# Kernel tuning notes

Measured on AMD Instinct MI355X. Metric: run time of the kernel, lower is better.

## Reference

```python
import jax, jax.numpy as jnp
import numpy as np

N_XI = 512      # internal REN state dim
L = 128         # nonlinearity channels (sequential loop length)
N_STATES = 128  # plant state dim (w)
N_INPUTS = 64   # control input dim (u)
EPS = 0.001
STD = 0.1
BATCH = 32768


def _model_params(X, Y):
    """set_model_param(): derive constrained REN matrices from free params X, Y."""
    n, l = N_XI, L
    H = X.T @ X + EPS * jnp.eye(2 * n + l, dtype=X.dtype)
    H11 = H[:n, :n]
    H21 = H[n:n + l, :n]
    H22 = H[n:n + l, n:n + l]
    H31 = H[n + l:, :n]
    H32 = H[n + l:, n:n + l]
    H33 = H[n + l:, n + l:]
    Fm = H31                                 # (n_xi, n_xi)
    B1 = H32                                 # (n_xi, l)
    E = 0.5 * (H11 + H33 + Y - Y.T)          # (n_xi, n_xi)
    Lam = 0.5 * jnp.diag(H22)                # (l,) strictly positive
    D11 = -jnp.tril(H22, -1)                 # strictly lower triangular (l, l)
    C1 = -H21                                # (l, n_xi)
    return Fm, B1, E, Lam, D11, C1


def setup_inputs() -> dict:
    key = jax.random.key(0)
    ks = jax.random.split(key, 9)
    n, l = N_XI, L
    return {
        "t": 0,
        "w": jax.random.normal(ks[0], (BATCH, 1, N_STATES), jnp.float32),
        "xi": jax.random.normal(ks[1], (BATCH, 1, n), jnp.float32),
        "X": jax.random.normal(ks[2], (2 * n + l, 2 * n + l), jnp.float32) * STD,
        "Y": jax.random.normal(ks[3], (n, n), jnp.float32) * STD,
        "B2": jax.random.normal(ks[4], (n, N_STATES), jnp.float32) * STD,
        "C2": jax.random.normal(ks[5], (N_INPUTS, n), jnp.float32) * STD,
        "D21": jax.random.normal(ks[6], (N_INPUTS, l), jnp.float32) * STD,
        "D22": jax.random.normal(ks[7], (N_INPUTS, N_STATES), jnp.float32) * STD,
        "D12": jax.random.normal(ks[8], (l, N_STATES), jnp.float32) * STD,
    }


def reference(t, w, xi, X, Y, B2, C2, D21, D22, D12):
    Fm, B1, E, Lam, D11, C1 = _model_params(X, Y)
    w2 = w[:, 0, :]    # (B, num_states)
    xi2 = xi[:, 0, :]  # (B, n_xi)

    # Precompute the xi- and w-dependent parts of every row's pre-activation.
    pre = xi2 @ C1.T + w2 @ D12.T  # (B, l)

    eye = jnp.eye(L, dtype=pre.dtype)

    def step(eps, xs):
        # Sequential forward substitution: row i only reads eps[:, :i]
        # because D11 is strictly lower triangular.
        d_row, p_col, lam, e_row = xs
        v = p_col + eps @ d_row            # (B,)
        e = jnp.tanh(v / lam)
        return eps + e[:, None] * e_row[None, :], None

    eps0 = jnp.zeros_like(pre)
    epsilon, _ = jax.lax.scan(step, eps0, (D11, pre.T, Lam, eye))  # (B, l)

    E_xi = xi2 @ Fm.T + epsilon @ B1.T + w2 @ B2.T      # (B, n_xi)
    xi_ = E_xi @ jnp.linalg.inv(E).T                    # (B, n_xi)
    u = xi2 @ C2.T + epsilon @ D21.T + w2 @ D22.T       # (B, num_inputs)
    return u[:, None, :], xi_[:, None, :]
```

## Files before the change

kernel.cpp:

```cpp
#include <hip/hip_runtime.h>
#include <cstddef>

#define NXI   512
#define LL    128
#define NST   128
#define NU    64
#define BATCH 32768
#define TW    1152
#define EPSC  0.001f
#define KC    768
#define NC    576
#define NCP   640

typedef unsigned short u16;
typedef __attribute__((ext_vector_type(8))) short   short8;
typedef __attribute__((ext_vector_type(4))) short   short4v;
typedef __attribute__((ext_vector_type(4))) float   f32x4;

__device__ __forceinline__ u16 f2bf(float f) {
    unsigned u = __float_as_uint(f);
    u += 0x7FFFu + ((u >> 16) & 1u);
    return (u16)(u >> 16);
}

__global__ __launch_bounds__(256) void k_setup(const float* __restrict__ X, u16* __restrict__ XT,
                                               const float* __restrict__ xi, const float* __restrict__ w,
                                               u16* __restrict__ Ac) {
    __shared__ float t[32][33];
    int blk = blockIdx.x;
    if (blk < 1296) {
        int tx = threadIdx.x & 31, ty = threadIdx.x >> 5;
        int bx = blk % 36, by = blk / 36;
        #pragma unroll
        for (int q = 0; q < 4; q++) {
            int r = ty + q * 8;
            t[r][tx] = X[(size_t)(by * 32 + r) * TW + bx * 32 + tx];
        }
        __syncthreads();
        #pragma unroll
        for (int q = 0; q < 4; q++) {
            int r = ty + q * 8;
            XT[(size_t)(bx * 32 + r) * TW + by * 32 + tx] = f2bf(t[tx][r]);
        }
        return;
    }
    size_t tt = (size_t)(blk - 1296) * 256 + threadIdx.x;
    int b = (int)(tt / 80), ch = (int)(tt % 80);
    const float* src;
    int col;
    if (ch < 64) { src = xi + (size_t)b * NXI + ch * 8;        col = ch * 8; }
    else         { src = w  + (size_t)b * NST + (ch - 64) * 8; col = 640 + (ch - 64) * 8; }
    f32x4 a = ((const f32x4*)src)[0], c = ((const f32x4*)src)[1];
    short8 o;
    o[0]=(short)f2bf(a[0]); o[1]=(short)f2bf(a[1]); o[2]=(short)f2bf(a[2]); o[3]=(short)f2bf(a[3]);
    o[4]=(short)f2bf(c[0]); o[5]=(short)f2bf(c[1]); o[6]=(short)f2bf(c[2]); o[7]=(short)f2bf(c[3]);
    *(short8*)(Ac + (size_t)b * KC + col) = o;
}

__global__ __launch_bounds__(256) void k_gemm2(const u16* __restrict__ A, int lda,
                                               const u16* __restrict__ W, int ldw,
                                               float* __restrict__ C0, int ldc0, int nsplit,
                                               float* __restrict__ C1, int ldc1,
                                               int K, int nbx, int ntrue, int swz) {
    __shared__ __align__(16) u16 As[2][128 * 32];
    __shared__ __align__(16) u16 Bs[2][128 * 32];
    int id = blockIdx.x;
    int bx, by;
    if (swz) {
        int j = id >> 3;
        int per = (int)(gridDim.x >> 3) / nbx;
        by = (id & 7) * per + j / nbx;
        bx = j - (j / nbx) * nbx;
    } else {
        by = id / nbx;
        bx = id - by * nbx;
    }
    const int tid = threadIdx.x;
    const int wave = tid >> 6, lane = tid & 63, quad = lane >> 4, l16 = lane & 15;
    const int bm0 = by * 128, bn0 = bx * 128;
    const int srow = tid >> 2;
    const int sch = (((tid & 3) ^ ((srow >> 2) & 3))) * 8;
    const u16* ga0 = A + (size_t)(bm0 + srow) * lda + sch;
    const u16* ga1 = ga0 + (size_t)64 * lda;
    const u16* gb0 = W + (size_t)(bn0 + srow) * ldw + sch;
    const u16* gb1 = gb0 + (size_t)64 * ldw;
    const int lo = wave * 512;
    const int mb = (wave >> 1) * 64, nb = (wave & 1) * 64;
    const int rch = (quad ^ (l16 >> 2)) * 8;

    f32x4 acc[4][4];
    #pragma unroll
    for (int i = 0; i < 4; i++)
        #pragma unroll
        for (int j = 0; j < 4; j++) acc[i][j] = (f32x4){0.f, 0.f, 0.f, 0.f};

    const int nk = K >> 5;
    __builtin_amdgcn_global_load_lds((void*)(ga0), (void*)(As[0] + lo),        16, 0, 0);
    __builtin_amdgcn_global_load_lds((void*)(ga1), (void*)(As[0] + lo + 2048), 16, 0, 0);
    __builtin_amdgcn_global_load_lds((void*)(gb0), (void*)(Bs[0] + lo),        16, 0, 0);
    __builtin_amdgcn_global_load_lds((void*)(gb1), (void*)(Bs[0] + lo + 2048), 16, 0, 0);
    __syncthreads();
    int cur = 0;
    for (int t = 0; t < nk; ++t) {
        if (t + 1 < nk) {
            const int kt = (t + 1) << 5;
            const int nx = cur ^ 1;
            __builtin_amdgcn_global_load_lds((void*)(ga0 + kt), (void*)(As[nx] + lo),        16, 0, 0);
            __builtin_amdgcn_global_load_lds((void*)(ga1 + kt), (void*)(As[nx] + lo + 2048), 16, 0, 0);
            __builtin_amdgcn_global_load_lds((void*)(gb0 + kt), (void*)(Bs[nx] + lo),        16, 0, 0);
            __builtin_amdgcn_global_load_lds((void*)(gb1 + kt), (void*)(Bs[nx] + lo + 2048), 16, 0, 0);
        }
        const u16* as = As[cur];
        const u16* bs = Bs[cur];
        short8 af[4], bf[4];
        #pragma unroll
        for (int mt = 0; mt < 4; mt++) af[mt] = *(const short8*)&as[(mb + mt * 16 + l16) * 32 + rch];
        #pragma unroll
        for (int nt = 0; nt < 4; nt++) bf[nt] = *(const short8*)&bs[(nb + nt * 16 + l16) * 32 + rch];
        #pragma unroll
        for (int mt = 0; mt < 4; mt++)
            #pragma unroll
            for (int nt = 0; nt < 4; nt++)
                acc[mt][nt] = __builtin_amdgcn_mfma_f32_16x16x32_bf16(af[mt], bf[nt], acc[mt][nt], 0, 0, 0);
        __syncthreads();
        cur ^= 1;
    }
    #pragma unroll
    for (int mt = 0; mt < 4; mt++)
        #pragma unroll
        for (int nt = 0; nt < 4; nt++)
            #pragma unroll
            for (int r = 0; r < 4; r++) {
                int row = bm0 + mb + mt * 16 + quad * 4 + r;
                int col = bn0 + nb + nt * 16 + l16;
                if (col < ntrue) {
                    float v = acc[mt][nt][r];
                    if (col < nsplit) C0[(size_t)row * ldc0 + col] = v;
                    else              C1[(size_t)row * ldc1 + (col - nsplit)] = v;
                }
            }
}

__global__ __launch_bounds__(256) void k_derive(const float* __restrict__ Hm, const float* __restrict__ Y,
                                                const float* __restrict__ B2, const float* __restrict__ D12,
                                                float* __restrict__ Agj, float* __restrict__ D11,
                                                float* __restrict__ rlam, u16* __restrict__ W1) {
    int idx = blockIdx.x * 256 + threadIdx.x;
    const int n0 = 512 * 1280, n1 = 128 * 128, n2 = 128, n3 = 128 * KC;
    if (idx < n0) {
        int i = idx / 1280, j = idx % 1280;
        float val;
        if (j < 512) {
            val = 0.5f * (Hm[(size_t)i * TW + j] + Hm[(size_t)(640 + i) * TW + 640 + j]
                          + Y[(size_t)i * 512 + j] - Y[(size_t)j * 512 + i]);
            if (i == j) val += EPSC;
        } else if (j < 1024) {
            val = Hm[(size_t)(640 + i) * TW + (j - 512)];
        } else if (j < 1152) {
            val = Hm[(size_t)(640 + i) * TW + 512 + (j - 1024)];
        } else {
            val = B2[(size_t)i * NST + (j - 1152)];
        }
        Agj[idx] = val;
        return;
    }
    idx -= n0;
    if (idx < n1) {
        int i = idx >> 7, j = idx & 127;
        D11[idx] = (j < i) ? -Hm[(size_t)(512 + i) * TW + 512 + j] : 0.f;
        return;
    }
    idx -= n1;
    if (idx < n2) {
        rlam[idx] = 2.0f / (Hm[(size_t)(512 + idx) * TW + 512 + idx] + EPSC);
        return;
    }
    idx -= n2;
    if (idx < n3) {
        int i = idx / KC, c = idx % KC;
        float v;
        if (c < 512)      v = -Hm[(size_t)(512 + i) * TW + c];
        else if (c < 640) v = 0.f;
        else              v = D12[(size_t)i * NST + (c - 640)];
        W1[(size_t)i * KC + c] = f2bf(v);
    }
}

__device__ __forceinline__ void invert64(float* Cl, float* Sa, float* Sb, float* mcol,
                                         float* rp, float* __restrict__ invOut, int tid) {
    int r = tid >> 2, c = tid & 3;
    float a[16], b[16];
    #pragma unroll
    for (int q = 0; q < 4; q++) {
        f32x4 v = *(f32x4*)&Cl[r * 68 + c * 16 + q * 4];
        a[q*4+0]=v[0]; a[q*4+1]=v[1]; a[q*4+2]=v[2]; a[q*4+3]=v[3];
    }
    #pragma unroll
    for (int j = 0; j < 16; j++) b[j] = (c * 16 + j == r) ? 1.f : 0.f;

    #pragma unroll
    for (int k = 0; k < 64; k++) {
        const int p = (k & 1) << 6;
        const int kc = k >> 4, kl = k & 15;
        if (r == k) {
            #pragma unroll
            for (int q = 0; q < 4; q++) {
                *(f32x4*)&Sa[p + c * 16 + q * 4] = (f32x4){a[q*4], a[q*4+1], a[q*4+2], a[q*4+3]};
                *(f32x4*)&Sb[p + c * 16 + q * 4] = (f32x4){b[q*4], b[q*4+1], b[q*4+2], b[q*4+3]};
            }
        }
        if (c == kc) {
            mcol[p + r] = a[kl];
            if (r == k) rp[k & 1] = 1.0f / a[kl];
        }
        __syncthreads();
        float m = (mcol[p + r] - ((r == k) ? 1.0f : 0.0f)) * rp[k & 1];
        #pragma unroll
        for (int q = 0; q < 4; q++) {
            f32x4 sa = *(f32x4*)&Sa[p + c * 16 + q * 4];
            f32x4 sb = *(f32x4*)&Sb[p + c * 16 + q * 4];
            a[q*4+0] = fmaf(-m, sa[0], a[q*4+0]); a[q*4+1] = fmaf(-m, sa[1], a[q*4+1]);
            a[q*4+2] = fmaf(-m, sa[2], a[q*4+2]); a[q*4+3] = fmaf(-m, sa[3], a[q*4+3]);
            b[q*4+0] = fmaf(-m, sb[0], b[q*4+0]); b[q*4+1] = fmaf(-m, sb[1], b[q*4+1]);
            b[q*4+2] = fmaf(-m, sb[2], b[q*4+2]); b[q*4+3] = fmaf(-m, sb[3], b[q*4+3]);
        }
    }
    #pragma unroll
    for (int q = 0; q < 4; q++)
        *(f32x4*)&invOut[r * 64 + c * 16 + q * 4] = (f32x4){b[q*4], b[q*4+1], b[q*4+2], b[q*4+3]};
}

__global__ __launch_bounds__(256) void k_diaginv0(const float* __restrict__ Agj, float* __restrict__ invD) {
    __shared__ __align__(16) float Cl[64 * 68];
    __shared__ float Sa[128], Sb[128], mcol[128], rp[2];
    int tid = threadIdx.x, r = tid >> 2, c4 = tid & 3;
    #pragma unroll
    for (int q = 0; q < 4; q++)
        *(f32x4*)&Cl[r * 68 + c4 * 16 + q * 4] = *(const f32x4*)(Agj + (size_t)r * 1280 + c4 * 16 + q * 4);
    __syncthreads();
    invert64(Cl, Sa, Sb, mcol, rp, invD, tid);
}

__global__ __launch_bounds__(256) void k_elim(float* __restrict__ Agj, float* __restrict__ invD, int k) {
    __shared__ __align__(16) float invDs[64 * 68];
    __shared__ __align__(16) float Ps[64 * 68];
    __shared__ __align__(16) float Ss[64 * 68];
    __shared__ __align__(16) float Ms[64 * 68];
    __shared__ float Sa[128], Sb[128], mcol[128], rp[2];
    int tid = threadIdx.x;
    int by = blockIdx.y, bx = blockIdx.x;
    int rb = by + (by >= k ? 1 : 0);
    int cb = k + 1 + bx;
    int lr = tid >> 2, lc = tid & 3;
    #pragma unroll
    for (int q = 0; q < 4; q++) {
        *(f32x4*)&invDs[lr * 68 + lc * 16 + q * 4] = *(const f32x4*)(invD + (size_t)k * 4096 + lr * 64 + lc * 16 + q * 4);
        *(f32x4*)&Ps[lr * 68 + lc * 16 + q * 4]    = *(const f32x4*)(Agj + (size_t)(k * 64 + lr) * 1280 + cb * 64 + lc * 16 + q * 4);
        *(f32x4*)&Ms[lr * 68 + lc * 16 + q * 4]    = *(const f32x4*)(Agj + (size_t)(rb * 64 + lr) * 1280 + k * 64 + lc * 16 + q * 4);
    }
    __syncthreads();
    int ty = tid >> 4, tx = tid & 15;
    f32x4 s[4];
    #pragma unroll
    for (int ri = 0; ri < 4; ri++) s[ri] = (f32x4){0.f, 0.f, 0.f, 0.f};
    for (int kk = 0; kk < 64; kk++) {
        f32x4 pv = *(f32x4*)&Ps[kk * 68 + tx * 4];
        #pragma unroll
        for (int ri = 0; ri < 4; ri++) s[ri] += pv * invDs[(ty * 4 + ri) * 68 + kk];
    }
    #pragma unroll
    for (int ri = 0; ri < 4; ri++) *(f32x4*)&Ss[(ty * 4 + ri) * 68 + tx * 4] = s[ri];
    __syncthreads();
    f32x4 accv[4];
    #pragma unroll
    for (int ri = 0; ri < 4; ri++)
        accv[ri] = *(const f32x4*)(Agj + (size_t)(rb * 64 + ty * 4 + ri) * 1280 + cb * 64 + tx * 4);
    for (int kk = 0; kk < 64; kk++) {
        f32x4 sv = *(f32x4*)&Ss[kk * 68 + tx * 4];
        #pragma unroll
        for (int ri = 0; ri < 4; ri++) accv[ri] -= sv * Ms[(ty * 4 + ri) * 68 + kk];
    }
    #pragma unroll
    for (int ri = 0; ri < 4; ri++)
        *(f32x4*)(Agj + (size_t)(rb * 64 + ty * 4 + ri) * 1280 + cb * 64 + tx * 4) = accv[ri];
    if (k < 7 && bx == 0 && by == k) {
        __syncthreads();
        #pragma unroll
        for (int ri = 0; ri < 4; ri++) *(f32x4*)&Ps[(ty * 4 + ri) * 68 + tx * 4] = accv[ri];
        __syncthreads();
        invert64(Ps, Sa, Sb, mcol, rp, invD + (size_t)(k + 1) * 4096, tid);
    }
}

__global__ __launch_bounds__(256) void k_finalize(const float* __restrict__ Agj, const float* __restrict__ invD,
                                                  const float* __restrict__ C2, const float* __restrict__ D21,
                                                  const float* __restrict__ D22, u16* __restrict__ Wc) {
    __shared__ __align__(16) float invDs[64 * 68];
    __shared__ __align__(16) float Ps[64 * 68];
    int tid = threadIdx.x, bx = blockIdx.x, by = blockIdx.y;
    int ty = tid >> 4, tx = tid & 15;
    if (by >= 8) {
        #pragma unroll
        for (int ri = 0; ri < 4; ri++) {
            int q = ty * 4 + ri;
            int row = 512 + (by - 8) * 64 + q;
            int cbase = bx * 64 + tx * 4;
            short4v o;
            if (by == 8) {
                f32x4 v;
                if (cbase < 512)      v = *(const f32x4*)(C2 + (size_t)q * 512 + cbase);
                else if (cbase < 640) v = *(const f32x4*)(D21 + (size_t)q * NST + (cbase - 512));
                else                  v = *(const f32x4*)(D22 + (size_t)q * NST + (cbase - 640));
                o[0]=(short)f2bf(v[0]); o[1]=(short)f2bf(v[1]); o[2]=(short)f2bf(v[2]); o[3]=(short)f2bf(v[3]);
            } else {
                o[0]=0; o[1]=0; o[2]=0; o[3]=0;
            }
            *(short4v*)(Wc + (size_t)row * KC + cbase) = o;
        }
        return;
    }
    int lr = tid >> 2, lc = tid & 3;
    #pragma unroll
    for (int q = 0; q < 4; q++) {
        *(f32x4*)&invDs[lr * 68 + lc * 16 + q * 4] = *(const f32x4*)(invD + (size_t)by * 4096 + lr * 64 + lc * 16 + q * 4);
        *(f32x4*)&Ps[lr * 68 + lc * 16 + q * 4]    = *(const f32x4*)(Agj + (size_t)(by * 64 + lr) * 1280 + 512 + bx * 64 + lc * 16 + q * 4);
    }
    __syncthreads();
    f32x4 s[4];
    #pragma unroll
    for (int ri = 0; ri < 4; ri++) s[ri] = (f32x4){0.f, 0.f, 0.f, 0.f};
    for (int kk = 0; kk < 64; kk++) {
        f32x4 pv = *(f32x4*)&Ps[kk * 68 + tx * 4];
        #pragma unroll
        for (int ri = 0; ri < 4; ri++) s[ri] += pv * invDs[(ty * 4 + ri) * 68 + kk];
    }
    #pragma unroll
    for (int ri = 0; ri < 4; ri++) {
        short4v o; o[0]=(short)f2bf(s[ri][0]); o[1]=(short)f2bf(s[ri][1]); o[2]=(short)f2bf(s[ri][2]); o[3]=(short)f2bf(s[ri][3]);
        *(short4v*)(Wc + (size_t)(by * 64 + ty * 4 + ri) * KC + bx * 64 + tx * 4) = o;
    }
}

__global__ __launch_bounds__(1024) void k_scan(const float* __restrict__ pre, const float* __restrict__ D11,
                                               const float* __restrict__ rlam, u16* __restrict__ Ac) {
    __shared__ __align__(16) float D11s[128 * 132];
    int tid = threadIdx.x;
    {
        int r = tid >> 3, c = (tid & 7) * 16;
        const f32x4* src = (const f32x4*)(D11 + (size_t)r * 128 + c);
        f32x4 v0 = src[0], v1 = src[1], v2 = src[2], v3 = src[3];
        f32x4* dst = (f32x4*)&D11s[r * 132 + c];
        dst[0] = v0; dst[1] = v1; dst[2] = v2; dst[3] = v3;
    }
    int lg = tid & 15;
    int row = blockIdx.x * 64 + (tid >> 4);
    int gbase = (tid & 63) & ~15;
    const float L2E2 = 2.885390082f;

    float corrv[8], a8[8];
    #pragma unroll
    for (int b = 0; b < 8; b++) {
        corrv[b] = pre[(size_t)row * 128 + b * 16 + lg];
        a8[b] = L2E2 * rlam[b * 16 + lg];
    }
    __syncthreads();

    #pragma unroll
    for (int b = 0; b < 8; b++) {
        f32x4 dblk[4];
        #pragma unroll
        for (int q = 0; q < 4; q++)
            dblk[q] = *(const f32x4*)&D11s[(b * 16 + lg) * 132 + b * 16 + q * 4];
        float v = corrv[b];
        float a = a8[b];
        float e16[16];
        float myeps = 0.f;
        #pragma unroll
        for (int t = 0; t < 16; t++) {
            float ex = __builtin_amdgcn_exp2f(a * v);
            float cand = 1.0f - 2.0f * __builtin_amdgcn_rcpf(ex + 1.0f);
            float e = __shfl(cand, gbase + t, 64);
            e16[t] = e;
            if (lg == t) myeps = e;
            v = fmaf(e, dblk[t >> 2][t & 3], v);
        }
        Ac[(size_t)row * KC + 512 + b * 16 + lg] = f2bf(myeps);
        #pragma unroll
        for (int bb = b + 1; bb < 8; bb++) {
            f32x4 dd[4];
            #pragma unroll
            for (int q = 0; q < 4; q++)
                dd[q] = *(const f32x4*)&D11s[(bb * 16 + lg) * 132 + b * 16 + q * 4];
            float acc = corrv[bb];
            #pragma unroll
            for (int t = 0; t < 16; t++)
                acc = fmaf(e16[t], dd[t >> 2][t & 3], acc);
            corrv[bb] = acc;
        }
    }
}

extern "C" void kernel_launch(void* const* d_in, const int* in_sizes, int n_in,
                              void* d_out, int out_size, void* d_ws, size_t ws_size,
                              hipStream_t stream) {
    const float* w_in  = (const float*)d_in[1];
    const float* xi_in = (const float*)d_in[2];
    const float* X   = (const float*)d_in[3];
    const float* Y   = (const float*)d_in[4];
    const float* B2  = (const float*)d_in[5];
    const float* C2  = (const float*)d_in[6];
    const float* D21 = (const float*)d_in[7];
    const float* D22 = (const float*)d_in[8];
    const float* D12 = (const float*)d_in[9];
    float* out_u  = (float*)d_out;
    float* out_xi = (float*)d_out + (size_t)BATCH * NU;

    char* base = (char*)d_ws;
    size_t off = 0;
    auto carve = [&](size_t bytes) -> void* {
        void* p = base + off;
        off += (bytes + 255) & ~(size_t)255;
        return p;
    };
    u16*   XT   = (u16*)  carve((size_t)TW * TW * 2);
    u16*   Ac   = (u16*)  carve((size_t)BATCH * KC * 2);
    float* Hm   = (float*)carve((size_t)TW * TW * 4);
    float* Agj  = (float*)carve((size_t)512 * 1280 * 4);
    float* invD = (float*)carve((size_t)8 * 64 * 64 * 4);
    u16*   Wc   = (u16*)  carve((size_t)NCP * KC * 2);
    u16*   W1   = (u16*)  carve((size_t)LL * KC * 2);
    float* pre  = (float*)carve((size_t)BATCH * LL * 4);
    float* D11  = (float*)carve((size_t)LL * LL * 4);
    float* rlam = (float*)carve((size_t)LL * 4);
    (void)ws_size; (void)in_sizes; (void)n_in; (void)out_size;

    k_setup<<<1296 + BATCH * 80 / 256, 256, 0, stream>>>(X, XT, xi_in, w_in, Ac);
    k_gemm2<<<81, 256, 0, stream>>>(XT, TW, XT, TW, Hm, TW, 1 << 30, nullptr, 0, TW, 9, TW, 0);
    k_derive<<<(512 * 1280 + 128 * 128 + 128 + 128 * KC + 255) / 256, 256, 0, stream>>>(
        Hm, Y, B2, D12, Agj, D11, rlam, W1);
    k_diaginv0<<<1, 256, 0, stream>>>(Agj, invD);
    for (int k = 0; k < 8; k++)
        k_elim<<<dim3(19 - k, 7), 256, 0, stream>>>(Agj, invD, k);
    k_finalize<<<dim3(12, 10), 256, 0, stream>>>(Agj, invD, C2, D21, D22, Wc);
    k_gemm2<<<256, 256, 0, stream>>>(Ac, KC, W1, KC, pre, LL, 1 << 30, nullptr, 0, KC, 1, LL, 1);
    k_scan<<<BATCH / 64, 1024, 0, stream>>>(pre, D11, rlam, Ac);
    k_gemm2<<<1280, 256, 0, stream>>>(Ac, KC, Wc, KC, out_xi, NXI, 512, out_u, NU, KC, 5, NC, 1);
}
```

Before: 517.9 us.

## Fuse Gauss-Jordan inverse stages into persistent kernel overlapped with pre GEMM

```diff
diff --git a/kernel.cpp b/kernel.cpp
--- a/kernel.cpp
+++ b/kernel.cpp
@@ -11,6 +11,7 @@
 #define KC    768
 #define NC    576
 #define NCP   640
+#define GJB   133
 
 typedef unsigned short u16;
 typedef __attribute__((ext_vector_type(8))) short   short8;
@@ -23,12 +24,33 @@
     return (u16)(u >> 16);
 }
 
+__device__ __forceinline__ void gbar(int* cnt, int* gen, int nblk) {
+    __syncthreads();
+    if (threadIdx.x == 0) {
+        int g = __hip_atomic_load(gen, __ATOMIC_RELAXED, __HIP_MEMORY_SCOPE_AGENT);
+        __threadfence();
+        if (__hip_atomic_fetch_add(cnt, 1, __ATOMIC_ACQ_REL, __HIP_MEMORY_SCOPE_AGENT) == nblk - 1) {
+            __hip_atomic_store(cnt, 0, __ATOMIC_RELAXED, __HIP_MEMORY_SCOPE_AGENT);
+            __hip_atomic_fetch_add(gen, 1, __ATOMIC_RELEASE, __HIP_MEMORY_SCOPE_AGENT);
+        } else {
+            int spins = 0;
+            while (__hip_atomic_load(gen, __ATOMIC_ACQUIRE, __HIP_MEMORY_SCOPE_AGENT) == g) {
+                __builtin_amdgcn_s_sleep(8);
+                if (++spins > (1 << 20)) break;
+            }
+        }
+        __threadfence();
+    }
+    __syncthreads();
+}
+
 __global__ __launch_bounds__(256) void k_setup(const float* __restrict__ X, u16* __restrict__ XT,
                                                const float* __restrict__ xi, const float* __restrict__ w,
-                                               u16* __restrict__ Ac) {
+                                               u16* __restrict__ Ac, int* __restrict__ bar) {
     __shared__ float t[32][33];
     int blk = blockIdx.x;
     if (blk < 1296) {
+        if (blk == 0 && threadIdx.x < 2) bar[threadIdx.x] = 0;
         int tx = threadIdx.x & 31, ty = threadIdx.x >> 5;
         int bx = blk % 36, by = blk / 36;
         #pragma unroll
@@ -230,114 +252,189 @@
         *(f32x4*)&invOut[r * 64 + c * 16 + q * 4] = (f32x4){b[q*4], b[q*4+1], b[q*4+2], b[q*4+3]};
 }
 
-__global__ __launch_bounds__(256) void k_diaginv0(const float* __restrict__ Agj, float* __restrict__ invD) {
-    __shared__ __align__(16) float Cl[64 * 68];
-    __shared__ float Sa[128], Sb[128], mcol[128], rp[2];
-    int tid = threadIdx.x, r = tid >> 2, c4 = tid & 3;
-    #pragma unroll
-    for (int q = 0; q < 4; q++)
-        *(f32x4*)&Cl[r * 68 + c4 * 16 + q * 4] = *(const f32x4*)(Agj + (size_t)r * 1280 + c4 * 16 + q * 4);
-    __syncthreads();
-    invert64(Cl, Sa, Sb, mcol, rp, invD, tid);
-}
-
-__global__ __launch_bounds__(256) void k_elim(float* __restrict__ Agj, float* __restrict__ invD, int k) {
-    __shared__ __align__(16) float invDs[64 * 68];
-    __shared__ __align__(16) float Ps[64 * 68];
-    __shared__ __align__(16) float Ss[64 * 68];
-    __shared__ __align__(16) float Ms[64 * 68];
-    __shared__ float Sa[128], Sb[128], mcol[128], rp[2];
-    int tid = threadIdx.x;
-    int by = blockIdx.y, bx = blockIdx.x;
-    int rb = by + (by >= k ? 1 : 0);
-    int cb = k + 1 + bx;
-    int lr = tid >> 2, lc = tid & 3;
-    #pragma unroll
-    for (int q = 0; q < 4; q++) {
-        *(f32x4*)&invDs[lr * 68 + lc * 16 + q * 4] = *(const f32x4*)(invD + (size_t)k * 4096 + lr * 64 + lc * 16 + q * 4);
-        *(f32x4*)&Ps[lr * 68 + lc * 16 + q * 4]    = *(const f32x4*)(Agj + (size_t)(k * 64 + lr) * 1280 + cb * 64 + lc * 16 + q * 4);
-        *(f32x4*)&Ms[lr * 68 + lc * 16 + q * 4]    = *(const f32x4*)(Agj + (size_t)(rb * 64 + lr) * 1280 + k * 64 + lc * 16 + q * 4);
-    }
-    __syncthreads();
-    int ty = tid >> 4, tx = tid & 15;
-    f32x4 s[4];
-    #pragma unroll
-    for (int ri = 0; ri < 4; ri++) s[ri] = (f32x4){0.f, 0.f, 0.f, 0.f};
-    for (int kk = 0; kk < 64; kk++) {
-        f32x4 pv = *(f32x4*)&Ps[kk * 68 + tx * 4];
-        #pragma unroll
-        for (int ri = 0; ri < 4; ri++) s[ri] += pv * invDs[(ty * 4 + ri) * 68 + kk];
-    }
-    #pragma unroll
-    for (int ri = 0; ri < 4; ri++) *(f32x4*)&Ss[(ty * 4 + ri) * 68 + tx * 4] = s[ri];
-    __syncthreads();
-    f32x4 accv[4];
-    #pragma unroll
-    for (int ri = 0; ri < 4; ri++)
-        accv[ri] = *(const f32x4*)(Agj + (size_t)(rb * 64 + ty * 4 + ri) * 1280 + cb * 64 + tx * 4);
-    for (int kk = 0; kk < 64; kk++) {
-        f32x4 sv = *(f32x4*)&Ss[kk * 68 + tx * 4];
-        #pragma unroll
-        for (int ri = 0; ri < 4; ri++) accv[ri] -= sv * Ms[(ty * 4 + ri) * 68 + kk];
-    }
-    #pragma unroll
-    for (int ri = 0; ri < 4; ri++)
-        *(f32x4*)(Agj + (size_t)(rb * 64 + ty * 4 + ri) * 1280 + cb * 64 + tx * 4) = accv[ri];
-    if (k < 7 && bx == 0 && by == k) {
+__global__ __launch_bounds__(256) void k_gj_fused(
+        float* __restrict__ Agj, float* __restrict__ invD,
+        const float* __restrict__ C2, const float* __restrict__ D21,
+        const float* __restrict__ D22, u16* __restrict__ Wc,
+        const u16* __restrict__ Ac, const u16* __restrict__ W1, float* __restrict__ pre,
+        int* __restrict__ bar) {
+    __shared__ __align__(16) float sm[4 * 4352 + 386];
+    const int tid = threadIdx.x;
+    const int id = blockIdx.x;
+
+    if (id >= GJB) {
+        u16* AsB = (u16*)sm;
+        u16* BsB = (u16*)sm + 8192;
+        const int by = id - GJB;
+        const int wave = tid >> 6, lane = tid & 63, quad = lane >> 4, l16 = lane & 15;
+        const int bm0 = by * 128;
+        const int srow = tid >> 2;
+        const int sch = (((tid & 3) ^ ((srow >> 2) & 3))) * 8;
+        const u16* ga0 = Ac + (size_t)(bm0 + srow) * KC + sch;
+        const u16* ga1 = ga0 + (size_t)64 * KC;
+        const u16* gb0 = W1 + (size_t)srow * KC + sch;
+        const u16* gb1 = gb0 + (size_t)64 * KC;
+        const int lo = wave * 512;
+        const int mb = (wave >> 1) * 64, nb = (wave & 1) * 64;
+        const int rch = (quad ^ (l16 >> 2)) * 8;
+        f32x4 acc[4][4];
+        #pragma unroll
+        for (int i = 0; i < 4; i++)
+            #pragma unroll
+            for (int j = 0; j < 4; j++) acc[i][j] = (f32x4){0.f, 0.f, 0.f, 0.f};
+        __builtin_amdgcn_global_load_lds((void*)(ga0), (void*)(AsB + lo),        16, 0, 0);
+        __builtin_amdgcn_global_load_lds((void*)(ga1), (void*)(AsB + lo + 2048), 16, 0, 0);
+        __builtin_amdgcn_global_load_lds((void*)(gb0), (void*)(BsB + lo),        16, 0, 0);
+        __builtin_amdgcn_global_load_lds((void*)(gb1), (void*)(BsB + lo + 2048), 16, 0, 0);
         __syncthreads();
-        #pragma unroll
-        for (int ri = 0; ri < 4; ri++) *(f32x4*)&Ps[(ty * 4 + ri) * 68 + tx * 4] = accv[ri];
+        int cur = 0;
+        for (int t = 0; t < 24; ++t) {
+            if (t + 1 < 24) {
+                const int kt = (t + 1) << 5;
+                const int nx = cur ^ 1;
+                __builtin_amdgcn_global_load_lds((void*)(ga0 + kt), (void*)(AsB + nx * 4096 + lo),        16, 0, 0);
+                __builtin_amdgcn_global_load_lds((void*)(ga1 + kt), (void*)(AsB + nx * 4096 + lo + 2048), 16, 0, 0);
+                __builtin_amdgcn_global_load_lds((void*)(gb0 + kt), (void*)(BsB + nx * 4096 + lo),        16, 0, 0);
+                __builtin_amdgcn_global_load_lds((void*)(gb1 + kt), (void*)(BsB + nx * 4096 + lo + 2048), 16, 0, 0);
+            }
+            const u16* as = AsB + cur * 4096;
+            const u16* bs = BsB + cur * 4096;
+            short8 af[4], bf[4];
+            #pragma unroll
+            for (int mt = 0; mt < 4; mt++) af[mt] = *(const short8*)&as[(mb + mt * 16 + l16) * 32 + rch];
+            #pragma unroll
+            for (int nt = 0; nt < 4; nt++) bf[nt] = *(const short8*)&bs[(nb + nt * 16 + l16) * 32 + rch];
+            #pragma unroll
+            for (int mt = 0; mt < 4; mt++)
+                #pragma unroll
+                for (int nt = 0; nt < 4; nt++)
+                    acc[mt][nt] = __builtin_amdgcn_mfma_f32_16x16x32_bf16(af[mt], bf[nt], acc[mt][nt], 0, 0, 0);
+            __syncthreads();
+            cur ^= 1;
+        }
+        #pragma unroll
+        for (int mt = 0; mt < 4; mt++)
+            #pragma unroll
+            for (int nt = 0; nt < 4; nt++)
+                #pragma unroll
+                for (int r = 0; r < 4; r++)
+                    pre[(size_t)(bm0 + mb + mt * 16 + quad * 4 + r) * LL + (nb + nt * 16 + l16)] = acc[mt][nt][r];
+        return;
+    }
+
+    float* invDs = sm;
+    float* Ps    = sm + 4352;
+    float* Ss    = sm + 8704;
+    float* Ms    = sm + 13056;
+    float* Sa    = sm + 17408;
+    float* Sb    = Sa + 128;
+    float* mcol  = Sb + 128;
+    float* rp    = mcol + 128;
+    int* cnt = bar;
+    int* gen = bar + 1;
+
+    if (id == 0) {
+        int r = tid >> 2, c4 = tid & 3;
+        #pragma unroll
+        for (int q = 0; q < 4; q++)
+            *(f32x4*)&Ps[r * 68 + c4 * 16 + q * 4] = *(const f32x4*)(Agj + (size_t)r * 1280 + c4 * 16 + q * 4);
         __syncthreads();
-        invert64(Ps, Sa, Sb, mcol, rp, invD + (size_t)(k + 1) * 4096, tid);
-    }
-}
-
-__global__ __launch_bounds__(256) void k_finalize(const float* __restrict__ Agj, const float* __restrict__ invD,
-                                                  const float* __restrict__ C2, const float* __restrict__ D21,
-                                                  const float* __restrict__ D22, u16* __restrict__ Wc) {
-    __shared__ __align__(16) float invDs[64 * 68];
-    __shared__ __align__(16) float Ps[64 * 68];
-    int tid = threadIdx.x, bx = blockIdx.x, by = blockIdx.y;
-    int ty = tid >> 4, tx = tid & 15;
-    if (by >= 8) {
+        invert64(Ps, Sa, Sb, mcol, rp, invD, tid);
+    }
+    gbar(cnt, gen, GJB);
+
+    for (int k = 0; k < 8; k++) {
+        const int nbk = 7 * (19 - k);
+        if (id < nbk) {
+            const int by = id % 7, bx = id / 7;
+            const int rb = by + (by >= k ? 1 : 0);
+            const int cb = k + 1 + bx;
+            int lr = tid >> 2, lc = tid & 3;
+            #pragma unroll
+            for (int q = 0; q < 4; q++) {
+                *(f32x4*)&invDs[lr * 68 + lc * 16 + q * 4] = *(const f32x4*)(invD + (size_t)k * 4096 + lr * 64 + lc * 16 + q * 4);
+                *(f32x4*)&Ps[lr * 68 + lc * 16 + q * 4]    = *(const f32x4*)(Agj + (size_t)(k * 64 + lr) * 1280 + cb * 64 + lc * 16 + q * 4);
+                *(f32x4*)&Ms[lr * 68 + lc * 16 + q * 4]    = *(const f32x4*)(Agj + (size_t)(rb * 64 + lr) * 1280 + k * 64 + lc * 16 + q * 4);
+            }
+            __syncthreads();
+            int ty = tid >> 4, tx = tid & 15;
+            f32x4 s[4];
+            #pragma unroll
+            for (int ri = 0; ri < 4; ri++) s[ri] = (f32x4){0.f, 0.f, 0.f, 0.f};
+            for (int kk = 0; kk < 64; kk++) {
+                f32x4 pv = *(f32x4*)&Ps[kk * 68 + tx * 4];
+                #pragma unroll
+                for (int ri = 0; ri < 4; ri++) s[ri] += pv * invDs[(ty * 4 + ri) * 68 + kk];
+            }
+            #pragma unroll
+            for (int ri = 0; ri < 4; ri++) *(f32x4*)&Ss[(ty * 4 + ri) * 68 + tx * 4] = s[ri];
+            __syncthreads();
+            f32x4 accv[4];
+            #pragma unroll
+            for (int ri = 0; ri < 4; ri++)
+                accv[ri] = *(const f32x4*)(Agj + (size_t)(rb * 64 + ty * 4 + ri) * 1280 + cb * 64 + tx * 4);
+            for (int kk = 0; kk < 64; kk++) {
+                f32x4 sv = *(f32x4*)&Ss[kk * 68 + tx * 4];
+                #pragma unroll
+                for (int ri = 0; ri < 4; ri++) accv[ri] -= sv * Ms[(ty * 4 + ri) * 68 + kk];
+            }
+            #pragma unroll
+            for (int ri = 0; ri < 4; ri++)
+                *(f32x4*)(Agj + (size_t)(rb * 64 + ty * 4 + ri) * 1280 + cb * 64 + tx * 4) = accv[ri];
+            if (k < 7 && bx == 0 && by == k) {
+                __syncthreads();
+                #pragma unroll
+                for (int ri = 0; ri < 4; ri++) *(f32x4*)&Ps[(ty * 4 + ri) * 68 + tx * 4] = accv[ri];
+                __syncthreads();
+                invert64(Ps, Sa, Sb, mcol, rp, invD + (size_t)(k + 1) * 4096, tid);
+            }
+        }
+        gbar(cnt, gen, GJB);
+    }
+
+    if (id < 120) {
+        const int bx = id % 12, by = id / 12;
+        int ty = tid >> 4, tx = tid & 15;
+        if (by >= 8) {
+            #pragma unroll
+            for (int ri = 0; ri < 4; ri++) {
+                int q = ty * 4 + ri;
+                int row = 512 + (by - 8) * 64 + q;
+                int cbase = bx * 64 + tx * 4;
+                short4v o;
+                if (by == 8) {
+                    f32x4 v;
+                    if (cbase < 512)      v = *(const f32x4*)(C2 + (size_t)q * 512 + cbase);
+                    else if (cbase < 640) v = *(const f32x4*)(D21 + (size_t)q * NST + (cbase - 512));
+                    else                  v = *(const f32x4*)(D22 + (size_t)q * NST + (cbase - 640));
+                    o[0]=(short)f2bf(v[0]); o[1]=(short)f2bf(v[1]); o[2]=(short)f2bf(v[2]); o[3]=(short)f2bf(v[3]);
+                } else {
+                    o[0]=0; o[1]=0; o[2]=0; o[3]=0;
+                }
+                *(short4v*)(Wc + (size_t)row * KC + cbase) = o;
+            }
+            return;
+        }
+        int lr = tid >> 2, lc = tid & 3;
+        #pragma unroll
+        for (int q = 0; q < 4; q++) {
+            *(f32x4*)&invDs[lr * 68 + lc * 16 + q * 4] = *(const f32x4*)(invD + (size_t)by * 4096 + lr * 64 + lc * 16 + q * 4);
+            *(f32x4*)&Ps[lr * 68 + lc * 16 + q * 4]    = *(const f32x4*)(Agj + (size_t)(by * 64 + lr) * 1280 + 512 + bx * 64 + lc * 16 + q * 4);
+        }
+        __syncthreads();
+        f32x4 s[4];
+        #pragma unroll
+        for (int ri = 0; ri < 4; ri++) s[ri] = (f32x4){0.f, 0.f, 0.f, 0.f};
+        for (int kk = 0; kk < 64; kk++) {
+            f32x4 pv = *(f32x4*)&Ps[kk * 68 + tx * 4];
+            #pragma unroll
+            for (int ri = 0; ri < 4; ri++) s[ri] += pv * invDs[(ty * 4 + ri) * 68 + kk];
+        }
         #pragma unroll
         for (int ri = 0; ri < 4; ri++) {
-            int q = ty * 4 + ri;
-            int row = 512 + (by - 8) * 64 + q;
-            int cbase = bx * 64 + tx * 4;
-            short4v o;
-            if (by == 8) {
-                f32x4 v;
-                if (cbase < 512)      v = *(const f32x4*)(C2 + (size_t)q * 512 + cbase);
-                else if (cbase < 640) v = *(const f32x4*)(D21 + (size_t)q * NST + (cbase - 512));
-                else                  v = *(const f32x4*)(D22 + (size_t)q * NST + (cbase - 640));
-                o[0]=(short)f2bf(v[0]); o[1]=(short)f2bf(v[1]); o[2]=(short)f2bf(v[2]); o[3]=(short)f2bf(v[3]);
-            } else {
-                o[0]=0; o[1]=0; o[2]=0; o[3]=0;
-            }
-            *(short4v*)(Wc + (size_t)row * KC + cbase) = o;
-        }
-        return;
-    }
-    int lr = tid >> 2, lc = tid & 3;
-    #pragma unroll
-    for (int q = 0; q < 4; q++) {
-        *(f32x4*)&invDs[lr * 68 + lc * 16 + q * 4] = *(const f32x4*)(invD + (size_t)by * 4096 + lr * 64 + lc * 16 + q * 4);
-        *(f32x4*)&Ps[lr * 68 + lc * 16 + q * 4]    = *(const f32x4*)(Agj + (size_t)(by * 64 + lr) * 1280 + 512 + bx * 64 + lc * 16 + q * 4);
-    }
-    __syncthreads();
-    f32x4 s[4];
-    #pragma unroll
-    for (int ri = 0; ri < 4; ri++) s[ri] = (f32x4){0.f, 0.f, 0.f, 0.f};
-    for (int kk = 0; kk < 64; kk++) {
-        f32x4 pv = *(f32x4*)&Ps[kk * 68 + tx * 4];
-        #pragma unroll
-        for (int ri = 0; ri < 4; ri++) s[ri] += pv * invDs[(ty * 4 + ri) * 68 + kk];
-    }
-    #pragma unroll
-    for (int ri = 0; ri < 4; ri++) {
-        short4v o; o[0]=(short)f2bf(s[ri][0]); o[1]=(short)f2bf(s[ri][1]); o[2]=(short)f2bf(s[ri][2]); o[3]=(short)f2bf(s[ri][3]);
-        *(short4v*)(Wc + (size_t)(by * 64 + ty * 4 + ri) * KC + bx * 64 + tx * 4) = o;
+            short4v o; o[0]=(short)f2bf(s[ri][0]); o[1]=(short)f2bf(s[ri][1]); o[2]=(short)f2bf(s[ri][2]); o[3]=(short)f2bf(s[ri][3]);
+            *(short4v*)(Wc + (size_t)(by * 64 + ty * 4 + ri) * KC + bx * 64 + tx * 4) = o;
+        }
     }
 }
 
@@ -432,17 +529,14 @@
     float* pre  = (float*)carve((size_t)BATCH * LL * 4);
     float* D11  = (float*)carve((size_t)LL * LL * 4);
     float* rlam = (float*)carve((size_t)LL * 4);
+    int*   bar  = (int*)  carve(256);
     (void)ws_size; (void)in_sizes; (void)n_in; (void)out_size;
 
-    k_setup<<<1296 + BATCH * 80 / 256, 256, 0, stream>>>(X, XT, xi_in, w_in, Ac);
+    k_setup<<<1296 + BATCH * 80 / 256, 256, 0, stream>>>(X, XT, xi_in, w_in, Ac, bar);
     k_gemm2<<<81, 256, 0, stream>>>(XT, TW, XT, TW, Hm, TW, 1 << 30, nullptr, 0, TW, 9, TW, 0);
     k_derive<<<(512 * 1280 + 128 * 128 + 128 + 128 * KC + 255) / 256, 256, 0, stream>>>(
         Hm, Y, B2, D12, Agj, D11, rlam, W1);
-    k_diaginv0<<<1, 256, 0, stream>>>(Agj, invD);
-    for (int k = 0; k < 8; k++)
-        k_elim<<<dim3(19 - k, 7), 256, 0, stream>>>(Agj, invD, k);
-    k_finalize<<<dim3(12, 10), 256, 0, stream>>>(Agj, invD, C2, D21, D22, Wc);
-    k_gemm2<<<256, 256, 0, stream>>>(Ac, KC, W1, KC, pre, LL, 1 << 30, nullptr, 0, KC, 1, LL, 1);
+    k_gj_fused<<<GJB + 256, 256, 0, stream>>>(Agj, invD, C2, D21, D22, Wc, Ac, W1, pre, bar);
     k_scan<<<BATCH / 64, 1024, 0, stream>>>(pre, D11, rlam, Ac);
     k_gemm2<<<1280, 256, 0, stream>>>(Ac, KC, Wc, KC, out_xi, NXI, 512, out_u, NU, KC, 5, NC, 1);
 }
```

After: 640.2 us. 23.6% more time.

## Fuse pre-activation GEMM into diag-inverse launch and use wave-level 64x64 inversion

Applied to the files above, without the earlier changes.

```diff
diff --git a/kernel.cpp b/kernel.cpp
--- a/kernel.cpp
+++ b/kernel.cpp
@@ -186,59 +186,99 @@
     }
 }
 
-__device__ __forceinline__ void invert64(float* Cl, float* Sa, float* Sb, float* mcol,
-                                         float* rp, float* __restrict__ invOut, int tid) {
-    int r = tid >> 2, c = tid & 3;
-    float a[16], b[16];
-    #pragma unroll
-    for (int q = 0; q < 4; q++) {
-        f32x4 v = *(f32x4*)&Cl[r * 68 + c * 16 + q * 4];
-        a[q*4+0]=v[0]; a[q*4+1]=v[1]; a[q*4+2]=v[2]; a[q*4+3]=v[3];
-    }
-    #pragma unroll
-    for (int j = 0; j < 16; j++) b[j] = (c * 16 + j == r) ? 1.f : 0.f;
-
-    #pragma unroll
-    for (int k = 0; k < 64; k++) {
-        const int p = (k & 1) << 6;
-        const int kc = k >> 4, kl = k & 15;
-        if (r == k) {
-            #pragma unroll
-            for (int q = 0; q < 4; q++) {
-                *(f32x4*)&Sa[p + c * 16 + q * 4] = (f32x4){a[q*4], a[q*4+1], a[q*4+2], a[q*4+3]};
-                *(f32x4*)&Sb[p + c * 16 + q * 4] = (f32x4){b[q*4], b[q*4+1], b[q*4+2], b[q*4+3]};
+__device__ __forceinline__ void inv64_core(float* a, int r) {
+    #pragma unroll
+    for (int k = 0; k < 64; ++k) {
+        float p  = __uint_as_float(__builtin_amdgcn_readlane(__float_as_uint(a[k]), k));
+        float ip = 1.0f / p;
+        float m  = a[k];
+        const bool piv = (r == k);
+        float tm = piv ? ip : -m * ip;
+        #pragma unroll
+        for (int j = 0; j < 64; ++j) {
+            float sj = __uint_as_float(__builtin_amdgcn_readlane(__float_as_uint(a[j]), k));
+            a[j] = fmaf(tm, sj, piv ? 0.f : a[j]);
+        }
+        a[k] = tm;
+    }
+}
+
+__global__ __launch_bounds__(256) void k_diaginv0(const float* __restrict__ Agj, float* __restrict__ invD,
+                                                  const u16* __restrict__ Ac, const u16* __restrict__ W1,
+                                                  float* __restrict__ pre) {
+    __shared__ __align__(16) u16 AsB[2][4096];
+    __shared__ __align__(16) u16 BsB[2][4096];
+    const int tid = threadIdx.x;
+    const int id = blockIdx.x;
+    if (id == 0) {
+        if (tid < 64) {
+            float a[64];
+            #pragma unroll
+            for (int j4 = 0; j4 < 16; ++j4) {
+                f32x4 v = *(const f32x4*)(Agj + (size_t)tid * 1280 + j4 * 4);
+                a[j4*4+0]=v[0]; a[j4*4+1]=v[1]; a[j4*4+2]=v[2]; a[j4*4+3]=v[3];
             }
-        }
-        if (c == kc) {
-            mcol[p + r] = a[kl];
-            if (r == k) rp[k & 1] = 1.0f / a[kl];
-        }
+            inv64_core(a, tid);
+            #pragma unroll
+            for (int j4 = 0; j4 < 16; ++j4)
+                *(f32x4*)(invD + (size_t)tid * 64 + j4 * 4) = (f32x4){a[j4*4], a[j4*4+1], a[j4*4+2], a[j4*4+3]};
+        }
+        return;
+    }
+    const int by = id - 1;
+    const int wave = tid >> 6, lane = tid & 63, quad = lane >> 4, l16 = lane & 15;
+    const int bm0 = by * 128;
+    const int srow = tid >> 2;
+    const int sch = (((tid & 3) ^ ((srow >> 2) & 3))) * 8;
+    const u16* ga0 = Ac + (size_t)(bm0 + srow) * KC + sch;
+    const u16* ga1 = ga0 + (size_t)64 * KC;
+    const u16* gb0 = W1 + (size_t)srow * KC + sch;
+    const u16* gb1 = gb0 + (size_t)64 * KC;
+    const int lo = wave * 512;
+    const int mb = (wave >> 1) * 64, nb = (wave & 1) * 64;
+    const int rch = (quad ^ (l16 >> 2)) * 8;
+    f32x4 acc[4][4];
+    #pragma unroll
+    for (int i = 0; i < 4; i++)
+        #pragma unroll
+        for (int j = 0; j < 4; j++) acc[i][j] = (f32x4){0.f, 0.f, 0.f, 0.f};
+    __builtin_amdgcn_global_load_lds((void*)(ga0), (void*)(AsB[0] + lo),        16, 0, 0);
+    __builtin_amdgcn_global_load_lds((void*)(ga1), (void*)(AsB[0] + lo + 2048), 16, 0, 0);
+    __builtin_amdgcn_global_load_lds((void*)(gb0), (void*)(BsB[0] + lo),        16, 0, 0);
+    __builtin_amdgcn_global_load_lds((void*)(gb1), (void*)(BsB[0] + lo + 2048), 16, 0, 0);
+    __syncthreads();
+    int cur = 0;
+    for (int t = 0; t < 24; ++t) {
+        if (t + 1 < 24) {
+            const int kt = (t + 1) << 5;
+            const int nx = cur ^ 1;
+            __builtin_amdgcn_global_load_lds((void*)(ga0 + kt), (void*)(AsB[nx] + lo),        16, 0, 0);
+            __builtin_amdgcn_global_load_lds((void*)(ga1 + kt), (void*)(AsB[nx] + lo + 2048), 16, 0, 0);
+            __builtin_amdgcn_global_load_lds((void*)(gb0 + kt), (void*)(BsB[nx] + lo),        16, 0, 0);
+            __builtin_amdgcn_global_load_lds((void*)(gb1 + kt), (void*)(BsB[nx] + lo + 2048), 16, 0, 0);
+        }
+        const u16* as = AsB[cur];
+        const u16* bs = BsB[cur];
+        short8 af[4], bf[4];
+        #pragma unroll
+        for (int mt = 0; mt < 4; mt++) af[mt] = *(const short8*)&as[(mb + mt * 16 + l16) * 32 + rch];
+        #pragma unroll
+        for (int nt = 0; nt < 4; nt++) bf[nt] = *(const short8*)&bs[(nb + nt * 16 + l16) * 32 + rch];
+        #pragma unroll
+        for (int mt = 0; mt < 4; mt++)
+            #pragma unroll
+            for (int nt = 0; nt < 4; nt++)
+                acc[mt][nt] = __builtin_amdgcn_mfma_f32_16x16x32_bf16(af[mt], bf[nt], acc[mt][nt], 0, 0, 0);
         __syncthreads();
-        float m = (mcol[p + r] - ((r == k) ? 1.0f : 0.0f)) * rp[k & 1];
-        #pragma unroll
-        for (int q = 0; q < 4; q++) {
-            f32x4 sa = *(f32x4*)&Sa[p + c * 16 + q * 4];
-            f32x4 sb = *(f32x4*)&Sb[p + c * 16 + q * 4];
-            a[q*4+0] = fmaf(-m, sa[0], a[q*4+0]); a[q*4+1] = fmaf(-m, sa[1], a[q*4+1]);
-            a[q*4+2] = fmaf(-m, sa[2], a[q*4+2]); a[q*4+3] = fmaf(-m, sa[3], a[q*4+3]);
-            b[q*4+0] = fmaf(-m, sb[0], b[q*4+0]); b[q*4+1] = fmaf(-m, sb[1], b[q*4+1]);
-            b[q*4+2] = fmaf(-m, sb[2], b[q*4+2]); b[q*4+3] = fmaf(-m, sb[3], b[q*4+3]);
-        }
-    }
-    #pragma unroll
-    for (int q = 0; q < 4; q++)
-        *(f32x4*)&invOut[r * 64 + c * 16 + q * 4] = (f32x4){b[q*4], b[q*4+1], b[q*4+2], b[q*4+3]};
-}
-
-__global__ __launch_bounds__(256) void k_diaginv0(const float* __restrict__ Agj, float* __restrict__ invD) {
-    __shared__ __align__(16) float Cl[64 * 68];
-    __shared__ float Sa[128], Sb[128], mcol[128], rp[2];
-    int tid = threadIdx.x, r = tid >> 2, c4 = tid & 3;
-    #pragma unroll
-    for (int q = 0; q < 4; q++)
-        *(f32x4*)&Cl[r * 68 + c4 * 16 + q * 4] = *(const f32x4*)(Agj + (size_t)r * 1280 + c4 * 16 + q * 4);
-    __syncthreads();
-    invert64(Cl, Sa, Sb, mcol, rp, invD, tid);
+        cur ^= 1;
+    }
+    #pragma unroll
+    for (int mt = 0; mt < 4; mt++)
+        #pragma unroll
+        for (int nt = 0; nt < 4; nt++)
+            #pragma unroll
+            for (int r = 0; r < 4; r++)
+                pre[(size_t)(bm0 + mb + mt * 16 + quad * 4 + r) * LL + (nb + nt * 16 + l16)] = acc[mt][nt][r];
 }
 
 __global__ __launch_bounds__(256) void k_elim(float* __restrict__ Agj, float* __restrict__ invD, int k) {
@@ -246,7 +286,6 @@
     __shared__ __align__(16) float Ps[64 * 68];
     __shared__ __align__(16) float Ss[64 * 68];
     __shared__ __align__(16) float Ms[64 * 68];
-    __shared__ float Sa[128], Sb[128], mcol[128], rp[2];
     int tid = threadIdx.x;
     int by = blockIdx.y, bx = blockIdx.x;
     int rb = by + (by >= k ? 1 : 0);
@@ -288,7 +327,19 @@
         #pragma unroll
         for (int ri = 0; ri < 4; ri++) *(f32x4*)&Ps[(ty * 4 + ri) * 68 + tx * 4] = accv[ri];
         __syncthreads();
-        invert64(Ps, Sa, Sb, mcol, rp, invD + (size_t)(k + 1) * 4096, tid);
+        if (tid < 64) {
+            float a[64];
+            #pragma unroll
+            for (int j4 = 0; j4 < 16; ++j4) {
+                f32x4 v = *(const f32x4*)&Ps[tid * 68 + j4 * 4];
+                a[j4*4+0]=v[0]; a[j4*4+1]=v[1]; a[j4*4+2]=v[2]; a[j4*4+3]=v[3];
+            }
+            inv64_core(a, tid);
+            #pragma unroll
+            for (int j4 = 0; j4 < 16; ++j4)
+                *(f32x4*)(invD + (size_t)(k + 1) * 4096 + (size_t)tid * 64 + j4 * 4) =
+                    (f32x4){a[j4*4], a[j4*4+1], a[j4*4+2], a[j4*4+3]};
+        }
     }
 }
 
@@ -438,11 +489,10 @@
     k_gemm2<<<81, 256, 0, stream>>>(XT, TW, XT, TW, Hm, TW, 1 << 30, nullptr, 0, TW, 9, TW, 0);
     k_derive<<<(512 * 1280 + 128 * 128 + 128 + 128 * KC + 255) / 256, 256, 0, stream>>>(
         Hm, Y, B2, D12, Agj, D11, rlam, W1);
-    k_diaginv0<<<1, 256, 0, stream>>>(Agj, invD);
+    k_diaginv0<<<257, 256, 0, stream>>>(Agj, invD, Ac, W1, pre);
     for (int k = 0; k < 8; k++)
         k_elim<<<dim3(19 - k, 7), 256, 0, stream>>>(Agj, invD, k);
     k_finalize<<<dim3(12, 10), 256, 0, stream>>>(Agj, invD, C2, D21, D22, Wc);
-    k_gemm2<<<256, 256, 0, stream>>>(Ac, KC, W1, KC, pre, LL, 1 << 30, nullptr, 0, KC, 1, LL, 1);
     k_scan<<<BATCH / 64, 1024, 0, stream>>>(pre, D11, rlam, Ac);
     k_gemm2<<<1280, 256, 0, stream>>>(Ac, KC, Wc, KC, out_xi, NXI, 512, out_u, NU, KC, 5, NC, 1);
 }
```

Result: slower. 1.389 ms (+168.1%).
